# Kernel tuning notes

Hardware: AMD Instinct MI355X
Metric: run time of the kernel (lower is better)

The kernel has to match this reference:

```python
import math
import jax, jax.numpy as jnp
import numpy as np

B, T, C = 4, 2048, 1024
H = 16
D = C // H  # head_dim = 64


def setup_inputs() -> dict:
    key = jax.random.key(0)
    ks = jax.random.split(key, 5)
    scale = 0.02
    return {
        "x": jax.random.normal(ks[0], (B, T, C), dtype=jnp.float32),
        "w_attn": jax.random.normal(ks[1], (C, 3 * C), dtype=jnp.float32) * scale,
        "b_attn": jax.random.normal(ks[2], (3 * C,), dtype=jnp.float32) * scale,
        "w_proj": jax.random.normal(ks[3], (C, C), dtype=jnp.float32) * scale,
        "b_proj": jax.random.normal(ks[4], (C,), dtype=jnp.float32) * scale,
    }


def reference(x, w_attn, b_attn, w_proj, b_proj):
    b, t, c = x.shape
    qkv = x @ w_attn + b_attn                       # [B,T,3C]
    q, k, v = jnp.split(qkv, 3, axis=-1)
    q = q.reshape(b, t, H, D)
    k = k.reshape(b, t, H, D)
    v = v.reshape(b, t, H, D)
    # scores: [B,H,T,T]
    att = jnp.einsum('bthd,bshd->bhts', q, k) * (1.0 / math.sqrt(D))
    causal = jnp.tril(jnp.ones((t, t), dtype=bool))
    att = jnp.where(causal, att, -jnp.inf)
    att = jax.nn.softmax(att, axis=-1)
    y = jnp.einsum('bhts,bshd->bthd', att, v).reshape(b, t, c)
    return y @ w_proj + b_proj
```

## Files before the change

kernel.cpp:

```cpp
#include <hip/hip_runtime.h>

#define BB 4
#define TT 2048
#define CC 1024
#define HH 16
#define DD 64
#define MM (BB*TT)
#define N3 (3*CC)
#define NTK 16

typedef unsigned short u16;
typedef __attribute__((ext_vector_type(8))) __bf16 bf16x8;
typedef __attribute__((ext_vector_type(4))) float f32x4;
typedef __attribute__((ext_vector_type(8))) u16 u16x8;
typedef __attribute__((ext_vector_type(4))) u16 u16x4;

__device__ __forceinline__ u16 f2bf(float f) {
  return __builtin_bit_cast(u16, (__bf16)f);
}

__device__ __forceinline__ void gload16(const void* g, void* lds) {
  __builtin_amdgcn_global_load_lds(
      (const __attribute__((address_space(1))) void*)g,
      (__attribute__((address_space(3))) void*)lds, 16, 0, 0);
}

__global__ __launch_bounds__(256) void k_cvt(const float* __restrict__ in, u16* __restrict__ out) {
  size_t i = ((size_t)blockIdx.x * 256 + threadIdx.x) * 8;
  f32x4 a = *(const f32x4*)(in + i);
  f32x4 b = *(const f32x4*)(in + i + 4);
  u16x8 o;
  o[0]=f2bf(a[0]); o[1]=f2bf(a[1]); o[2]=f2bf(a[2]); o[3]=f2bf(a[3]);
  o[4]=f2bf(b[0]); o[5]=f2bf(b[1]); o[6]=f2bf(b[2]); o[7]=f2bf(b[3]);
  *(u16x8*)(out + i) = o;
}

__global__ __launch_bounds__(256) void k_tr(const float* __restrict__ in, u16* __restrict__ out,
                                            int R, int Cc) {
  __shared__ float t[32][33];
  int cb = blockIdx.x * 32, rb = blockIdx.y * 32;
  int tx = threadIdx.x, ty = threadIdx.y;
  #pragma unroll
  for (int j = 0; j < 4; ++j)
    t[ty + j*8][tx] = in[(size_t)(rb + ty + j*8) * Cc + cb + tx];
  __syncthreads();
  #pragma unroll
  for (int j = 0; j < 4; ++j)
    out[(size_t)(cb + ty + j*8) * R + rb + tx] = f2bf(t[tx][ty + j*8]);
}

__device__ __forceinline__ void gemm_ring(const u16* __restrict__ A, const u16* __restrict__ Bt,
                                          int mbase, int nbase,
                                          u16 (*As)[128*64], u16 (*Bs)[256*64],
                                          f32x4 acc[4][4]) {
  int tid = threadIdx.x;
  int lane = tid & 63;
  int wid = tid >> 6;
  int wm = (wid >> 2) * 64, wn = (wid & 3) * 64;
  int r = lane & 15, g = lane >> 4;

  auto STAGE = [&](int sl, int u) {
    int kb = u * 64;
    #pragma unroll
    for (int i = 0; i < 2; ++i) {
      int c = tid + 512*i;
      int row = c >> 3, ch = c & 7;
      int chs = ch ^ (row & 7);
      gload16(A + (size_t)(mbase + row)*CC + kb + chs*8, &As[sl][c*8]);
    }
    #pragma unroll
    for (int i = 0; i < 4; ++i) {
      int c = tid + 512*i;
      int row = c >> 3, ch = c & 7;
      int chs = ch ^ (row & 7);
      gload16(Bt + (size_t)(nbase + row)*CC + kb + chs*8, &Bs[sl][c*8]);
    }
  };

  STAGE(0, 0);
  STAGE(1, 1);
  asm volatile("s_waitcnt vmcnt(6)" ::: "memory");
  __builtin_amdgcn_s_barrier();

  int sl = 0;
  for (int u = 0; u < NTK; ++u) {
    int s2 = sl + 2; if (s2 >= 3) s2 -= 3;
    if (u + 2 < NTK) STAGE(s2, u + 2);

    bf16x8 af[2][4], bfr[2][4];
    #pragma unroll
    for (int ks = 0; ks < 2; ++ks) {
      #pragma unroll
      for (int mi = 0; mi < 4; ++mi)
        af[ks][mi] = *(const bf16x8*)&As[sl][(wm + mi*16 + r)*64 + (((ks*4 + g) ^ (r & 7)) << 3)];
      #pragma unroll
      for (int ni = 0; ni < 4; ++ni)
        bfr[ks][ni] = *(const bf16x8*)&Bs[sl][(wn + ni*16 + r)*64 + (((ks*4 + g) ^ (r & 7)) << 3)];
    }
    #pragma unroll
    for (int ks = 0; ks < 2; ++ks)
      #pragma unroll
      for (int mi = 0; mi < 4; ++mi)
        #pragma unroll
        for (int ni = 0; ni < 4; ++ni)
          acc[mi][ni] = __builtin_amdgcn_mfma_f32_16x16x32_bf16(af[ks][mi], bfr[ks][ni], acc[mi][ni], 0, 0, 0);

    if (u + 2 < NTK) asm volatile("s_waitcnt vmcnt(6)" ::: "memory");
    else             asm volatile("s_waitcnt vmcnt(0)" ::: "memory");
    __builtin_amdgcn_s_barrier();
    ++sl; if (sl >= 3) sl -= 3;
  }
}

__device__ __forceinline__ void grid_map(int bid, int& bx, int& by) {
  int xcd = bid & 7;
  int idx = bid >> 3;
  bx = xcd * 8 + (idx & 7);
  by = idx >> 3;
}

__global__ __launch_bounds__(512) void k_gemm_qkv(const u16* __restrict__ Xb, const u16* __restrict__ WaT,
                                                  const float* __restrict__ b_attn,
                                                  u16* __restrict__ Qh, u16* __restrict__ Kh,
                                                  u16* __restrict__ Vt) {
  __shared__ u16 As[3][128*64];
  __shared__ u16 Bs[3][256*64];
  f32x4 acc[4][4] = {};
  int bx, by; grid_map(blockIdx.x, bx, by);
  int mbase = bx * 128, nbase = by * 256;
  gemm_ring(Xb, WaT, mbase, nbase, As, Bs, acc);
  int lane = threadIdx.x & 63, wid = threadIdx.x >> 6;
  int wm = (wid >> 2) * 64, wn = (wid & 3) * 64;
  int r = lane & 15, g = lane >> 4;
  int which = nbase >> 10;
  if (which < 2) {
    u16* dst = which == 0 ? Qh : Kh;
    #pragma unroll
    for (int mi = 0; mi < 4; ++mi)
      #pragma unroll
      for (int ni = 0; ni < 4; ++ni)
        #pragma unroll
        for (int reg = 0; reg < 4; ++reg) {
          int m = mbase + wm + mi*16 + 4*g + reg;
          int n = nbase + wn + ni*16 + r;
          float v = acc[mi][ni][reg] + b_attn[n];
          int ccol = n & (CC - 1);
          int h = ccol >> 6, d = ccol & 63;
          int bb = m >> 11, t = m & (TT - 1);
          dst[((size_t)(bb*HH + h)*TT + t)*DD + d] = f2bf(v);
        }
  } else {
    #pragma unroll
    for (int mi = 0; mi < 4; ++mi)
      #pragma unroll
      for (int ni = 0; ni < 4; ++ni) {
        int m0 = mbase + wm + mi*16 + 4*g;
        int n = nbase + wn + ni*16 + r;
        float bn = b_attn[n];
        int ccol = n & (CC - 1);
        int h = ccol >> 6, d = ccol & 63;
        int bb = m0 >> 11, t0 = m0 & (TT - 1);
        u16x4 pk;
        #pragma unroll
        for (int reg = 0; reg < 4; ++reg)
          pk[reg] = f2bf(acc[mi][ni][reg] + bn);
        *(u16x4*)&Vt[((size_t)(bb*HH + h)*DD + d)*TT + t0] = pk;
      }
  }
}

__global__ __launch_bounds__(512) void k_gemm_proj(const u16* __restrict__ Yh, const u16* __restrict__ WpT,
                                                   const float* __restrict__ b_proj,
                                                   float* __restrict__ out) {
  __shared__ u16 As[3][128*64];
  __shared__ u16 Bs[3][256*64];
  f32x4 acc[4][4] = {};
  int bx, by; grid_map(blockIdx.x, bx, by);
  int mbase = bx * 128, nbase = by * 256;
  gemm_ring(Yh, WpT, mbase, nbase, As, Bs, acc);
  int lane = threadIdx.x & 63, wid = threadIdx.x >> 6;
  int wm = (wid >> 2) * 64, wn = (wid & 3) * 64;
  int r = lane & 15, g = lane >> 4;
  #pragma unroll
  for (int mi = 0; mi < 4; ++mi)
    #pragma unroll
    for (int ni = 0; ni < 4; ++ni)
      #pragma unroll
      for (int reg = 0; reg < 4; ++reg) {
        int m = mbase + wm + mi*16 + 4*g + reg;
        int n = nbase + wn + ni*16 + r;
        out[(size_t)m*CC + n] = acc[mi][ni][reg] + b_proj[n];
      }
}

__global__ __launch_bounds__(256) void k_attn(const u16* __restrict__ Qh, const u16* __restrict__ Kh,
                                              const u16* __restrict__ Vtg, u16* __restrict__ Yh) {
  __shared__ u16 Ks[2][64*64];
  __shared__ u16 Vs[2][64*64];
  __shared__ u16 Pl[4][32*64];
  int bid = blockIdx.x;
  int bh = (bid & 7) * 8 + (bid >> 6);
  int p  = (bid >> 3) & 7;
  int b = bh >> 4, h = bh & 15;
  int tid = threadIdx.x, lane = tid & 63, w = tid >> 6;
  int r = lane & 15, g = lane >> 4;
  size_t hoff = (size_t)bh * TT * DD;
  u16* pw = Pl[w];

  bf16x8 ones;
  #pragma unroll
  for (int e = 0; e < 8; ++e) ones[e] = (__bf16)1.0f;

  auto STAGE = [&](int buf, int kb) {
    #pragma unroll
    for (int i = 0; i < 2; ++i) {
      int c = tid + 256*i;
      int row = c >> 3, ch = c & 7;
      int chs = ch ^ (row & 7);
      gload16(Kh  + hoff + (size_t)(kb*64 + row)*DD + chs*8, &Ks[buf][c*8]);
      gload16(Vtg + hoff + (size_t)row*TT + kb*64 + chs*8,   &Vs[buf][c*8]);
    }
  };

  for (int ph = 0; ph < 2; ++ph) {
    int qt = ph == 0 ? (15 - p) : p;
    int qrow0 = qt*128 + w*32;
    int nkb = 2*qt + 2;

    bf16x8 qf[2][2];
    #pragma unroll
    for (int ni = 0; ni < 2; ++ni)
      #pragma unroll
      for (int ks = 0; ks < 2; ++ks)
        qf[ni][ks] = *(const bf16x8*)(Qh + hoff + (size_t)(qrow0 + ni*16 + r)*DD + ks*32 + g*8);

    f32x4 o[2][4] = {};
    f32x4 lacc[2] = {};

    STAGE(0, 0);
    __syncthreads();
    int buf = 0;

    for (int kb = 0; kb < nkb; ++kb) {
      if (kb + 1 < nkb) STAGE(buf ^ 1, kb + 1);

      if (kb*64 <= qrow0 + 31) {
        f32x4 s[2][4] = {};
        __builtin_amdgcn_s_setprio(1);
        #pragma unroll
        for (int nf = 0; nf < 4; ++nf)
          #pragma unroll
          for (int ks = 0; ks < 2; ++ks) {
            bf16x8 kf = *(const bf16x8*)&Ks[buf][(nf*16 + r)*64 + (((ks*4 + g) ^ (r & 7)) << 3)];
            #pragma unroll
            for (int ni = 0; ni < 2; ++ni)
              s[ni][nf] = __builtin_amdgcn_mfma_f32_16x16x32_bf16(kf, qf[ni][ks], s[ni][nf], 0, 0, 0);
          }
        __builtin_amdgcn_s_setprio(0);
        bool need_mask = (kb*64 + 63 > qrow0);
        #pragma unroll
        for (int ni = 0; ni < 2; ++ni)
          #pragma unroll
          for (int nf = 0; nf < 4; ++nf)
            #pragma unroll
            for (int reg = 0; reg < 4; ++reg) {
              float sv = s[ni][nf][reg] * 0.18033688011112043f;
              if (need_mask) {
                int key = kb*64 + nf*16 + 4*g + reg;
                int qrow = qrow0 + ni*16 + r;
                sv = (key > qrow) ? -1e30f : sv;
              }
              s[ni][nf][reg] = __builtin_amdgcn_exp2f(sv);
            }
        #pragma unroll
        for (int ni = 0; ni < 2; ++ni)
          #pragma unroll
          for (int nf = 0; nf < 4; ++nf) {
            int qh_ = ni*16 + r;
            int chunk = 2*nf + (g >> 1);
            u16x4 pk;
            #pragma unroll
            for (int reg = 0; reg < 4; ++reg) pk[reg] = f2bf(s[ni][nf][reg]);
            *(u16x4*)&pw[qh_*64 + ((chunk ^ (qh_ & 7)) << 3) + ((g & 1) << 2)] = pk;
          }
        __builtin_amdgcn_s_setprio(1);
        #pragma unroll
        for (int ks = 0; ks < 2; ++ks) {
          bf16x8 pb[2];
          #pragma unroll
          for (int ni = 0; ni < 2; ++ni)
            pb[ni] = *(const bf16x8*)&pw[(ni*16 + r)*64 + (((ks*4 + g) ^ (r & 7)) << 3)];
          #pragma unroll
          for (int nf2 = 0; nf2 < 4; ++nf2) {
            bf16x8 vf = *(const bf16x8*)&Vs[buf][(nf2*16 + r)*64 + (((ks*4 + g) ^ (r & 7)) << 3)];
            #pragma unroll
            for (int ni = 0; ni < 2; ++ni)
              o[ni][nf2] = __builtin_amdgcn_mfma_f32_16x16x32_bf16(vf, pb[ni], o[ni][nf2], 0, 0, 0);
          }
          #pragma unroll
          for (int ni = 0; ni < 2; ++ni)
            lacc[ni] = __builtin_amdgcn_mfma_f32_16x16x32_bf16(ones, pb[ni], lacc[ni], 0, 0, 0);
        }
        __builtin_amdgcn_s_setprio(0);
      }
      __syncthreads();
      buf ^= 1;
    }

    #pragma unroll
    for (int ni = 0; ni < 2; ++ni) {
      float inv = 1.0f / lacc[ni][0];
      int t = qrow0 + ni*16 + r;
      #pragma unroll
      for (int nf2 = 0; nf2 < 4; ++nf2) {
        u16x4 pk;
        #pragma unroll
        for (int reg = 0; reg < 4; ++reg)
          pk[reg] = f2bf(o[ni][nf2][reg] * inv);
        *(u16x4*)&Yh[((size_t)b*TT + t)*CC + h*DD + nf2*16 + 4*g] = pk;
      }
    }
  }
}

extern "C" void kernel_launch(void* const* d_in, const int* in_sizes, int n_in,
                              void* d_out, int out_size, void* d_ws, size_t ws_size,
                              hipStream_t stream) {
  const float* x      = (const float*)d_in[0];
  const float* w_attn = (const float*)d_in[1];
  const float* b_attn = (const float*)d_in[2];
  const float* w_proj = (const float*)d_in[3];
  const float* b_proj = (const float*)d_in[4];
  float* out = (float*)d_out;

  u16* Xb  = (u16*)d_ws;
  u16* WaT = Xb  + (size_t)MM*CC;
  u16* WpT = WaT + (size_t)N3*CC;
  u16* Qh  = WpT + (size_t)CC*CC;
  u16* Kh  = Qh  + (size_t)BB*HH*TT*DD;
  u16* Vt  = Kh  + (size_t)BB*HH*TT*DD;
  u16* Yh  = Vt  + (size_t)BB*HH*TT*DD;

  k_cvt<<<dim3(MM*CC/(256*8)), dim3(256), 0, stream>>>(x, Xb);
  k_tr <<<dim3(N3/32, CC/32), dim3(32,8), 0, stream>>>(w_attn, WaT, CC, N3);
  k_tr <<<dim3(CC/32, CC/32), dim3(32,8), 0, stream>>>(w_proj, WpT, CC, CC);
  k_gemm_qkv<<<dim3((MM/128)*(N3/256)), dim3(512), 0, stream>>>(Xb, WaT, b_attn, Qh, Kh, Vt);
  k_attn<<<dim3(BB*HH*8), dim3(256), 0, stream>>>(Qh, Kh, Vt, Yh);
  k_gemm_proj<<<dim3((MM/128)*(CC/256)), dim3(512), 0, stream>>>(Yh, WpT, b_proj, out);
}
```

Before: 188.8 us.

## Split GEMM k-tile into two phases interleaving prefetch, LDS reads and prioritized MFMA

Restructures the shared GEMM main loop into two half-k phases. Each phase issues part of the next-stage global-to-LDS prefetch, reads its fragments, syncs with extra barriers, and runs its MFMAs at raised wave priority. The goal is to overlap memory issue with compute better and to halve fragment register pressure. The cost is four barriers per k-tile instead of one, which adds synchronization overhead.

```diff
diff --git a/kernel.cpp b/kernel.cpp
--- a/kernel.cpp
+++ b/kernel.cpp
@@ -59,7 +59,7 @@
   int wm = (wid >> 2) * 64, wn = (wid & 3) * 64;
   int r = lane & 15, g = lane >> 4;
 
-  auto STAGE = [&](int sl, int u) {
+  auto STAGE_A = [&](int sl, int u) {
     int kb = u * 64;
     #pragma unroll
     for (int i = 0; i < 2; ++i) {
@@ -68,46 +68,53 @@
       int chs = ch ^ (row & 7);
       gload16(A + (size_t)(mbase + row)*CC + kb + chs*8, &As[sl][c*8]);
     }
-    #pragma unroll
-    for (int i = 0; i < 4; ++i) {
-      int c = tid + 512*i;
-      int row = c >> 3, ch = c & 7;
-      int chs = ch ^ (row & 7);
-      gload16(Bt + (size_t)(nbase + row)*CC + kb + chs*8, &Bs[sl][c*8]);
-    }
   };
-
-  STAGE(0, 0);
-  STAGE(1, 1);
+  auto STAGE_B1 = [&](int sl, int u, int i) {
+    int kb = u * 64;
+    int c = tid + 512*i;
+    int row = c >> 3, ch = c & 7;
+    int chs = ch ^ (row & 7);
+    gload16(Bt + (size_t)(nbase + row)*CC + kb + chs*8, &Bs[sl][c*8]);
+  };
+
+  STAGE_A(0, 0); STAGE_B1(0, 0, 0); STAGE_B1(0, 0, 1); STAGE_B1(0, 0, 2); STAGE_B1(0, 0, 3);
+  STAGE_A(1, 1); STAGE_B1(1, 1, 0); STAGE_B1(1, 1, 1); STAGE_B1(1, 1, 2); STAGE_B1(1, 1, 3);
   asm volatile("s_waitcnt vmcnt(6)" ::: "memory");
   __builtin_amdgcn_s_barrier();
 
   int sl = 0;
   for (int u = 0; u < NTK; ++u) {
     int s2 = sl + 2; if (s2 >= 3) s2 -= 3;
-    if (u + 2 < NTK) STAGE(s2, u + 2);
-
-    bf16x8 af[2][4], bfr[2][4];
+    bool pre = (u + 2 < NTK);
     #pragma unroll
     for (int ks = 0; ks < 2; ++ks) {
+      if (pre) {
+        if (ks == 0) { STAGE_A(s2, u + 2); STAGE_B1(s2, u + 2, 0); }
+        else         { STAGE_B1(s2, u + 2, 1); STAGE_B1(s2, u + 2, 2); STAGE_B1(s2, u + 2, 3); }
+      }
+      bf16x8 af[4], bfr[4];
       #pragma unroll
       for (int mi = 0; mi < 4; ++mi)
-        af[ks][mi] = *(const bf16x8*)&As[sl][(wm + mi*16 + r)*64 + (((ks*4 + g) ^ (r & 7)) << 3)];
+        af[mi]  = *(const bf16x8*)&As[sl][(wm + mi*16 + r)*64 + (((ks*4 + g) ^ (r & 7)) << 3)];
       #pragma unroll
       for (int ni = 0; ni < 4; ++ni)
-        bfr[ks][ni] = *(const bf16x8*)&Bs[sl][(wn + ni*16 + r)*64 + (((ks*4 + g) ^ (r & 7)) << 3)];
-    }
-    #pragma unroll
-    for (int ks = 0; ks < 2; ++ks)
+        bfr[ni] = *(const bf16x8*)&Bs[sl][(wn + ni*16 + r)*64 + (((ks*4 + g) ^ (r & 7)) << 3)];
+      __builtin_amdgcn_s_barrier();
+      asm volatile("s_waitcnt lgkmcnt(0)" ::: "memory");
+      __builtin_amdgcn_sched_barrier(0);
+      __builtin_amdgcn_s_setprio(1);
       #pragma unroll
       for (int mi = 0; mi < 4; ++mi)
         #pragma unroll
         for (int ni = 0; ni < 4; ++ni)
-          acc[mi][ni] = __builtin_amdgcn_mfma_f32_16x16x32_bf16(af[ks][mi], bfr[ks][ni], acc[mi][ni], 0, 0, 0);
-
-    if (u + 2 < NTK) asm volatile("s_waitcnt vmcnt(6)" ::: "memory");
-    else             asm volatile("s_waitcnt vmcnt(0)" ::: "memory");
-    __builtin_amdgcn_s_barrier();
+          acc[mi][ni] = __builtin_amdgcn_mfma_f32_16x16x32_bf16(af[mi], bfr[ni], acc[mi][ni], 0, 0, 0);
+      __builtin_amdgcn_s_setprio(0);
+      if (ks == 1) {
+        if (pre) asm volatile("s_waitcnt vmcnt(6)" ::: "memory");
+        else     asm volatile("s_waitcnt vmcnt(0)" ::: "memory");
+      }
+      __builtin_amdgcn_s_barrier();
+    }
     ++sl; if (sl >= 3) sl -= 3;
   }
 }
```

Measured after the change: 209.3 us. 1.11x slower.
